# Kernel optimization log

Hardware: AMD Instinct MI355X
Metric: run time of the kernel (lower is better)

Reference implementation:

```python
import jax, jax.numpy as jnp
import numpy as np

B, G, N, E, F, H = 16, 8, 512, 8192, 128, 128
BN_EPS = 1e-5


def setup_inputs() -> dict:
    key = jax.random.key(0)
    ks = jax.random.split(key, 6)
    feats = jax.random.normal(ks[0], (B, G, N, F), jnp.float32)
    edges = jax.random.randint(ks[1], (B, G, 2, E), 0, N, dtype=jnp.int32)
    s = lambda k, shape: jax.random.normal(k, shape, jnp.float32) * 0.05
    return {
        "feats": feats,
        "edges": edges,
        "W0": s(ks[2], (F, H)), "b0": jnp.zeros((H,), jnp.float32),
        "W1": s(ks[3], (H, H)), "b1": jnp.zeros((H,), jnp.float32),
        "Wt": s(ks[4], (H, H)), "bt": jnp.zeros((H,), jnp.float32),
        "gamma": jnp.ones((H,), jnp.float32),
        "beta": jnp.zeros((H,), jnp.float32),
        "run_mean": jnp.zeros((H,), jnp.float32),
        "run_var": jnp.ones((H,), jnp.float32),
    }


def _gconv(x, src, dst, W, b):
    # DGL GraphConv with norm='both': relu(D_in^{-1/2} A D_out^{-1/2} X W + b)
    ones = jnp.ones(src.shape, jnp.float32)
    out_deg = jnp.clip(jax.ops.segment_sum(ones, src, num_segments=N), 1.0)
    in_deg = jnp.clip(jax.ops.segment_sum(ones, dst, num_segments=N), 1.0)
    h = x * jax.lax.rsqrt(out_deg)[:, None]          # src normalization
    agg = jax.ops.segment_sum(h[src], dst, num_segments=N)  # SpMM gather+scatter
    h = agg * jax.lax.rsqrt(in_deg)[:, None]          # dst normalization
    return jax.nn.relu(h @ W + b)


def reference(feats, edges, W0, b0, W1, b1, Wt, bt, gamma, beta, run_mean, run_var):
    def per_graph(x, e):
        src, dst = e[0], e[1]
        h = _gconv(x, src, dst, W0, b0)
        h = _gconv(h, src, dst, W1, b1)
        emb = h.mean(axis=0)  # dgl.mean_nodes readout -> [H]
        z = emb @ Wt + bt
        # BatchNorm1d in eval mode (batch of 1 graph embedding)
        z = gamma * (z - run_mean) * jax.lax.rsqrt(run_var + BN_EPS) + beta
        return jax.nn.relu(z)

    xf = feats.reshape(B * G, N, F)
    ef = edges.reshape(B * G, 2, E)
    out = jax.vmap(per_graph)(xf, ef)  # [B*G, H]
    # torch.stack nesting gives (batch, n_graph, 1, H) since mean_nodes returns [1, H]
    return out.reshape(B, G, 1, H)
```

## Files before the change

kernel.cpp:

```cpp
#include <hip/hip_runtime.h>
#include <hip/hip_bf16.h>

#define NN 512
#define NE 8192
#define NG 128
#define FH 128
#define APITCH 68
#define XPITCH 136
#define BN_EPS 1e-5f

typedef __attribute__((ext_vector_type(8))) short s8v;
typedef __attribute__((ext_vector_type(4))) float f4v;
typedef __attribute__((ext_vector_type(4))) unsigned short us4v;

__device__ inline unsigned short f2bf(float x) {
    unsigned u = __float_as_uint(x);
    unsigned r = (u + 0x7fffu + ((u >> 16) & 1u)) >> 16;
    return (unsigned short)r;
}
__device__ inline float bf2f(unsigned short h) { return __uint_as_float(((unsigned)h) << 16); }

__global__ __launch_bounds__(1024) void k_build(const int* __restrict__ edges,
                                                float* __restrict__ rs_out,
                                                float* __restrict__ rs_in,
                                                int* __restrict__ row_ofs,
                                                int* __restrict__ csr_src,
                                                int* __restrict__ csr_dst,
                                                const float* __restrict__ W0,
                                                const float* __restrict__ W1,
                                                unsigned short* __restrict__ WP) {
    int g = blockIdx.x;
    int tid = threadIdx.x;

    if (g >= NG) {
        int which = g - NG;
        const float* W = which ? W1 : W0;
        for (int task = tid; task < 2048; task += 1024) {
            int t = task >> 6;
            int lane = task & 63;
            int nt = t >> 2, kk = t & 3;
            int n = nt * 16 + (lane & 15);
            int k0 = kk * 32 + (lane >> 4) * 8;
            unsigned short* dh = WP + ((size_t)which * 2 + 0) * 16384 + ((size_t)t * 64 + lane) * 8;
            unsigned short* dl = WP + ((size_t)which * 2 + 1) * 16384 + ((size_t)t * 64 + lane) * 8;
#pragma unroll
            for (int j = 0; j < 8; j++) {
                float v = W[(size_t)(k0 + j) * FH + n];
                unsigned short h = f2bf(v);
                dh[j] = h;
                dl[j] = f2bf(v - bf2f(h));
            }
        }
        return;
    }

    const int* src = edges + (size_t)g * 2 * NE;
    const int* dst = src + NE;

    __shared__ int degO[NN], degI[NN];
    __shared__ int scanA[NN], scanB[NN];
    __shared__ int fill[NN];
    __shared__ int csr_lds[NE];
    __shared__ int dst_lds[NE];

    for (int i = tid; i < NN; i += 1024) { degO[i] = 0; degI[i] = 0; }
    __syncthreads();
    for (int u = tid; u < NE / 4; u += 1024) {
        int4 s = ((const int4*)src)[u];
        int4 d = ((const int4*)dst)[u];
        atomicAdd(&degO[s.x], 1); atomicAdd(&degO[s.y], 1);
        atomicAdd(&degO[s.z], 1); atomicAdd(&degO[s.w], 1);
        atomicAdd(&degI[d.x], 1); atomicAdd(&degI[d.y], 1);
        atomicAdd(&degI[d.z], 1); atomicAdd(&degI[d.w], 1);
    }
    __syncthreads();
    for (int i = tid; i < NN; i += 1024) {
        int dO = degO[i], dI = degI[i];
        rs_out[g * NN + i] = rsqrtf((float)max(dO, 1));
        rs_in [g * NN + i] = rsqrtf((float)max(dI, 1));
        scanA[i] = dI;
    }
    __syncthreads();
    int* sA = scanA; int* sB = scanB;
    for (int off = 1; off < NN; off <<= 1) {
        for (int i = tid; i < NN; i += 1024) {
            int v = sA[i];
            if (i >= off) v += sA[i - off];
            sB[i] = v;
        }
        __syncthreads();
        int* t = sA; sA = sB; sB = t;
    }
    for (int i = tid; i < NN; i += 1024) {
        int excl = (i == 0) ? 0 : sA[i - 1];
        fill[i] = excl;
        row_ofs[g * 513 + i] = excl;
    }
    if (tid == 0) row_ofs[g * 513 + NN] = sA[NN - 1];
    __syncthreads();
    for (int u = tid; u < NE / 4; u += 1024) {
        int4 s = ((const int4*)src)[u];
        int4 d = ((const int4*)dst)[u];
        int p0 = atomicAdd(&fill[d.x], 1); csr_lds[p0] = s.x; dst_lds[p0] = d.x;
        int p1 = atomicAdd(&fill[d.y], 1); csr_lds[p1] = s.y; dst_lds[p1] = d.y;
        int p2 = atomicAdd(&fill[d.z], 1); csr_lds[p2] = s.z; dst_lds[p2] = d.z;
        int p3 = atomicAdd(&fill[d.w], 1); csr_lds[p3] = s.w; dst_lds[p3] = d.w;
    }
    __syncthreads();
    for (int u = tid; u < NE / 4; u += 1024) {
        ((int4*)(csr_src + (size_t)g * NE))[u] = ((const int4*)csr_lds)[u];
        ((int4*)(csr_dst + (size_t)g * NE))[u] = ((const int4*)dst_lds)[u];
    }
}

__global__ __launch_bounds__(256) void k_gemm_f32(const float* __restrict__ X,
                                                  const unsigned short* __restrict__ WPh,
                                                  const unsigned short* __restrict__ WPl,
                                                  const float* __restrict__ rs,
                                                  unsigned short* __restrict__ Yf) {
    __shared__ unsigned short xh[64 * XPITCH];
    __shared__ unsigned short xl[64 * XPITCH];
    int tid = threadIdx.x;
    int sb = blockIdx.y;
    size_t r0 = (size_t)blockIdx.x * NN + (size_t)sb * 64;

    const float4* Xv = (const float4*)(X + r0 * FH);
#pragma unroll
    for (int i = 0; i < 8; i++) {
        int u = tid + i * 256;
        int row = u >> 5, c4 = (u & 31) * 4;
        float4 v = Xv[u];
        int off = row * XPITCH + c4;
        unsigned short h0 = f2bf(v.x), h1 = f2bf(v.y), h2 = f2bf(v.z), h3 = f2bf(v.w);
        xh[off + 0] = h0; xh[off + 1] = h1; xh[off + 2] = h2; xh[off + 3] = h3;
        xl[off + 0] = f2bf(v.x - bf2f(h0));
        xl[off + 1] = f2bf(v.y - bf2f(h1));
        xl[off + 2] = f2bf(v.z - bf2f(h2));
        xl[off + 3] = f2bf(v.w - bf2f(h3));
    }
    __syncthreads();

    int lane = tid & 63, w = tid >> 6;
    int quad = lane >> 4, m = lane & 15;
    int arow = w * 16 + m;

    f4v acc[8];
#pragma unroll
    for (int nt = 0; nt < 8; nt++) acc[nt] = (f4v){0.f, 0.f, 0.f, 0.f};

#pragma unroll
    for (int kk = 0; kk < 4; kk++) {
        s8v ah = *(const s8v*)&xh[arow * XPITCH + kk * 32 + quad * 8];
        s8v al = *(const s8v*)&xl[arow * XPITCH + kk * 32 + quad * 8];
#pragma unroll
        for (int nt = 0; nt < 8; nt++) {
            s8v bh = *(const s8v*)(WPh + ((size_t)(nt * 4 + kk) * 64 + lane) * 8);
            s8v bl = *(const s8v*)(WPl + ((size_t)(nt * 4 + kk) * 64 + lane) * 8);
            acc[nt] = __builtin_amdgcn_mfma_f32_16x16x32_bf16(ah, bh, acc[nt], 0, 0, 0);
            acc[nt] = __builtin_amdgcn_mfma_f32_16x16x32_bf16(al, bh, acc[nt], 0, 0, 0);
            acc[nt] = __builtin_amdgcn_mfma_f32_16x16x32_bf16(ah, bl, acc[nt], 0, 0, 0);
        }
    }

    int orow = w * 16 + quad * 4;
    float4 rsv = *(const float4*)(rs + r0 + orow);
    int tag = (w * 2 + (quad >> 1)) & 3;
    int kko = sb * 2 + (w >> 1);
    int j0  = (quad & 1) * 4;
    unsigned short* of = Yf + (size_t)blockIdx.x * (NN * FH);
#pragma unroll
    for (int nt = 0; nt < 8; nt++) {
        us4v v;
        v.x = f2bf(acc[nt][0] * rsv.x);
        v.y = f2bf(acc[nt][1] * rsv.y);
        v.z = f2bf(acc[nt][2] * rsv.z);
        v.w = f2bf(acc[nt][3] * rsv.w);
        *(us4v*)(of + (((size_t)kko * 8 + nt) * 64 + (m + 16 * tag)) * 8 + j0) = v;
    }
}

__global__ __launch_bounds__(512) void k_fused(const unsigned short* __restrict__ Y1f,
                                               const int* __restrict__ row_ofs,
                                               const int* __restrict__ csr_src,
                                               const int* __restrict__ csr_dst,
                                               const float* __restrict__ rs_in,
                                               const float* __restrict__ rs_out,
                                               const float* __restrict__ bias,
                                               const unsigned short* __restrict__ WPh,
                                               const unsigned short* __restrict__ WPl,
                                               unsigned short* __restrict__ Y2f) {
    int g  = blockIdx.x;
    int sb = blockIdx.y;
    int tid = threadIdx.x;
    int lane = tid & 63, w8 = tid >> 6;
    int quad = lane >> 4, m = lane & 15;
    int mt = w8 & 3, nh = w8 >> 2;
    int base = sb * 64;

    __shared__ int Ach[64 * APITCH];
    __shared__ unsigned short Bs[2 * 8 * 64 * 8];
    unsigned short* hs = (unsigned short*)Ach;
    __shared__ float rsin_s[64];

    if (tid < 64) rsin_s[tid] = rs_in[g * NN + base + tid];

    int eS = row_ofs[g * 513 + base];
    int eE = row_ofs[g * 513 + base + 64];
    const int* cs = csr_src + (size_t)g * NE;
    const int* cd = csr_dst + (size_t)g * NE;
    const int4* Yi4 = (const int4*)(Y1f + (size_t)g * (NN * FH));
    int4* Bi4 = (int4*)Bs;

    f4v acc[4];
#pragma unroll
    for (int j = 0; j < 4; j++) acc[j] = (f4v){0.f, 0.f, 0.f, 0.f};

    for (int p = 0; p < 8; p++) {
        __syncthreads();
        for (int i = tid; i < 64 * APITCH; i += 512) Ach[i] = 0;
        __syncthreads();
        for (int e = eS + tid; e < eE; e += 512) {
            int s = cs[e], d = cd[e];
            if ((s >> 6) == p) atomicAdd(&Ach[(d - base) * APITCH + (s & 63)], 1);
        }
        for (int u = tid; u < 1024; u += 512) Bi4[u] = Yi4[p * 1024 + u];
        __syncthreads();
#pragma unroll
        for (int kkl = 0; kkl < 2; kkl++) {
            s8v bf[4];
#pragma unroll
            for (int j = 0; j < 4; j++)
                bf[j] = *(const s8v*)&Bs[((kkl * 8 + nh * 4 + j) * 64 + lane) * 8];
            const int* ap = &Ach[(mt * 16 + m) * APITCH + kkl * 32 + quad * 8];
            int4 a0 = *(const int4*)ap;
            int4 a1 = *(const int4*)(ap + 4);
            s8v af;
            af[0] = (short)f2bf((float)a0.x); af[1] = (short)f2bf((float)a0.y);
            af[2] = (short)f2bf((float)a0.z); af[3] = (short)f2bf((float)a0.w);
            af[4] = (short)f2bf((float)a1.x); af[5] = (short)f2bf((float)a1.y);
            af[6] = (short)f2bf((float)a1.z); af[7] = (short)f2bf((float)a1.w);
#pragma unroll
            for (int j = 0; j < 4; j++)
                acc[j] = __builtin_amdgcn_mfma_f32_16x16x32_bf16(af, bf[j], acc[j], 0, 0, 0);
        }
    }
    __syncthreads();

#pragma unroll
    for (int j = 0; j < 4; j++) {
        int feat = (nh * 4 + j) * 16 + m;
        float bv = bias[feat];
#pragma unroll
        for (int i = 0; i < 4; i++) {
            int r = mt * 16 + quad * 4 + i;
            float hv = fmaxf(fmaf(rsin_s[r], acc[j][i], bv), 0.f);
            hs[r * XPITCH + feat] = f2bf(hv);
        }
    }
    __syncthreads();

    f4v acc2[4];
#pragma unroll
    for (int j = 0; j < 4; j++) acc2[j] = (f4v){0.f, 0.f, 0.f, 0.f};

#pragma unroll
    for (int kk = 0; kk < 4; kk++) {
        s8v ah = *(const s8v*)&hs[(mt * 16 + m) * XPITCH + kk * 32 + quad * 8];
#pragma unroll
        for (int j = 0; j < 4; j++) {
            int nt = nh * 4 + j;
            s8v bh = *(const s8v*)(WPh + ((size_t)(nt * 4 + kk) * 64 + lane) * 8);
            s8v bl = *(const s8v*)(WPl + ((size_t)(nt * 4 + kk) * 64 + lane) * 8);
            acc2[j] = __builtin_amdgcn_mfma_f32_16x16x32_bf16(ah, bh, acc2[j], 0, 0, 0);
            acc2[j] = __builtin_amdgcn_mfma_f32_16x16x32_bf16(ah, bl, acc2[j], 0, 0, 0);
        }
    }

    int orow = mt * 16 + quad * 4;
    float4 rsv = *(const float4*)(rs_out + (size_t)g * NN + base + orow);
    int tag = (mt * 2 + (quad >> 1)) & 3;
    int kko = sb * 2 + (mt >> 1);
    int j0  = (quad & 1) * 4;
    unsigned short* of = Y2f + (size_t)g * (NN * FH);
#pragma unroll
    for (int j = 0; j < 4; j++) {
        int nt = nh * 4 + j;
        us4v v;
        v.x = f2bf(acc2[j][0] * rsv.x);
        v.y = f2bf(acc2[j][1] * rsv.y);
        v.z = f2bf(acc2[j][2] * rsv.z);
        v.w = f2bf(acc2[j][3] * rsv.w);
        *(us4v*)(of + (((size_t)kko * 8 + nt) * 64 + (m + 16 * tag)) * 8 + j0) = v;
    }
}

__global__ __launch_bounds__(512) void k_gather_mean(const unsigned short* __restrict__ Y2f,
                                                     const int* __restrict__ row_ofs,
                                                     const int* __restrict__ csr_src,
                                                     const int* __restrict__ csr_dst,
                                                     const float* __restrict__ rs_in,
                                                     const float* __restrict__ bias,
                                                     float* __restrict__ partial) {
    int g  = blockIdx.x;
    int sb = blockIdx.y;
    int tid = threadIdx.x;
    int lane = tid & 63, w8 = tid >> 6;
    int quad = lane >> 4, m = lane & 15;
    int mt = w8 & 3, nh = w8 >> 2;
    int base = sb * 64;

    __shared__ int Ach[64 * APITCH];
    __shared__ unsigned short Bs[2 * 8 * 64 * 8];
    float* red = (float*)Ach;
    __shared__ float rsin_s[64];

    if (tid < 64) rsin_s[tid] = rs_in[g * NN + base + tid];

    int eS = row_ofs[g * 513 + base];
    int eE = row_ofs[g * 513 + base + 64];
    const int* cs = csr_src + (size_t)g * NE;
    const int* cd = csr_dst + (size_t)g * NE;
    const int4* Yi4 = (const int4*)(Y2f + (size_t)g * (NN * FH));
    int4* Bi4 = (int4*)Bs;

    f4v acc[4];
#pragma unroll
    for (int j = 0; j < 4; j++) acc[j] = (f4v){0.f, 0.f, 0.f, 0.f};

    for (int p = 0; p < 8; p++) {
        __syncthreads();
        for (int i = tid; i < 64 * APITCH; i += 512) Ach[i] = 0;
        __syncthreads();
        for (int e = eS + tid; e < eE; e += 512) {
            int s = cs[e], d = cd[e];
            if ((s >> 6) == p) atomicAdd(&Ach[(d - base) * APITCH + (s & 63)], 1);
        }
        for (int u = tid; u < 1024; u += 512) Bi4[u] = Yi4[p * 1024 + u];
        __syncthreads();
#pragma unroll
        for (int kkl = 0; kkl < 2; kkl++) {
            s8v bf[4];
#pragma unroll
            for (int j = 0; j < 4; j++)
                bf[j] = *(const s8v*)&Bs[((kkl * 8 + nh * 4 + j) * 64 + lane) * 8];
            const int* ap = &Ach[(mt * 16 + m) * APITCH + kkl * 32 + quad * 8];
            int4 a0 = *(const int4*)ap;
            int4 a1 = *(const int4*)(ap + 4);
            s8v af;
            af[0] = (short)f2bf((float)a0.x); af[1] = (short)f2bf((float)a0.y);
            af[2] = (short)f2bf((float)a0.z); af[3] = (short)f2bf((float)a0.w);
            af[4] = (short)f2bf((float)a1.x); af[5] = (short)f2bf((float)a1.y);
            af[6] = (short)f2bf((float)a1.z); af[7] = (short)f2bf((float)a1.w);
#pragma unroll
            for (int j = 0; j < 4; j++)
                acc[j] = __builtin_amdgcn_mfma_f32_16x16x32_bf16(af, bf[j], acc[j], 0, 0, 0);
        }
    }
    __syncthreads();

#pragma unroll
    for (int j = 0; j < 4; j++) {
        int feat = (nh * 4 + j) * 16 + m;
        float bv = bias[feat];
        float s = 0.f;
#pragma unroll
        for (int i = 0; i < 4; i++) {
            int r = mt * 16 + quad * 4 + i;
            s += fmaxf(fmaf(rsin_s[r], acc[j][i], bv), 0.f);
        }
        red[(w8 * 64 + lane) * 4 + j] = s;
    }
    __syncthreads();
    if (tid < FH) {
        int f = tid;
        int nt = f >> 4, mm = f & 15;
        int nhh = nt >> 2, jj = nt & 3;
        float t = 0.f;
#pragma unroll
        for (int mtt = 0; mtt < 4; mtt++)
#pragma unroll
            for (int q = 0; q < 4; q++)
                t += red[(((nhh * 4 + mtt) * 64) + q * 16 + mm) * 4 + jj];
        partial[((size_t)g * 8 + sb) * FH + f] = t;
    }
}

__global__ __launch_bounds__(128) void k_head(const float* __restrict__ partial,
                                              const float* __restrict__ Wt,
                                              const float* __restrict__ bt,
                                              const float* __restrict__ gamma,
                                              const float* __restrict__ beta,
                                              const float* __restrict__ rmean,
                                              const float* __restrict__ rvar,
                                              float* __restrict__ out) {
    int g = blockIdx.x;
    int j = threadIdx.x;
    __shared__ float e[FH];
    float acc8 = 0.f;
#pragma unroll
    for (int q = 0; q < 8; q++) acc8 += partial[((size_t)g * 8 + q) * FH + j];
    e[j] = acc8 * (1.0f / (float)NN);
    __syncthreads();
    float acc = bt[j];
#pragma unroll 8
    for (int k = 0; k < FH; k++) acc += e[k] * Wt[(size_t)k * FH + j];
    float z = gamma[j] * (acc - rmean[j]) * rsqrtf(rvar[j] + BN_EPS) + beta[j];
    out[g * FH + j] = fmaxf(z, 0.f);
}

extern "C" void kernel_launch(void* const* d_in, const int* in_sizes, int n_in,
                              void* d_out, int out_size, void* d_ws, size_t ws_size,
                              hipStream_t stream) {
    const float* feats = (const float*)d_in[0];
    const int*   edges = (const int*)d_in[1];
    const float* W0    = (const float*)d_in[2];
    const float* b0    = (const float*)d_in[3];
    const float* W1    = (const float*)d_in[4];
    const float* b1    = (const float*)d_in[5];
    const float* Wt    = (const float*)d_in[6];
    const float* bt    = (const float*)d_in[7];
    const float* gamma = (const float*)d_in[8];
    const float* beta  = (const float*)d_in[9];
    const float* rmean = (const float*)d_in[10];
    const float* rvar  = (const float*)d_in[11];
    float* out = (float*)d_out;

    char* w = (char*)d_ws;
    float* rs_out  = (float*)w;   w += sizeof(float) * NG * NN;
    float* rs_in   = (float*)w;   w += sizeof(float) * NG * NN;
    int*   row_ofs = (int*)w;     w += sizeof(int) * NG * 520;
    int*   csr_src = (int*)w;     w += sizeof(int) * ((size_t)NG * NE + 16);
    int*   csr_dst = (int*)w;     w += sizeof(int) * ((size_t)NG * NE + 16);
    unsigned short* WP = (unsigned short*)w;  w += sizeof(unsigned short) * 4 * 16384;
    unsigned short* Y1 = (unsigned short*)w;  w += sizeof(unsigned short) * (size_t)NG * NN * FH;
    unsigned short* Y2 = (unsigned short*)w;  w += sizeof(unsigned short) * (size_t)NG * NN * FH;
    float* partial = (float*)w;   w += sizeof(float) * NG * 8 * FH;

    unsigned short* WPh0 = WP;
    unsigned short* WPl0 = WP + 16384;
    unsigned short* WPh1 = WP + 32768;
    unsigned short* WPl1 = WP + 49152;

    k_build<<<NG + 2, 1024, 0, stream>>>(edges, rs_out, rs_in, row_ofs, csr_src, csr_dst,
                                         W0, W1, WP);

    k_gemm_f32<<<dim3(NG, 8), 256, 0, stream>>>(feats, WPh0, WPl0, rs_out, Y1);

    k_fused<<<dim3(NG, 8), 512, 0, stream>>>(Y1, row_ofs, csr_src, csr_dst,
                                             rs_in, rs_out, b0, WPh1, WPl1, Y2);

    k_gather_mean<<<dim3(NG, 8), 512, 0, stream>>>(Y2, row_ofs, csr_src, csr_dst, rs_in, b1, partial);

    k_head<<<NG, 128, 0, stream>>>(partial, Wt, bt, gamma, beta, rmean, rvar, out);

    (void)in_sizes; (void)n_in; (void)out_size; (void)ws_size;
}
```

Measured before the change: 185.9 us.

## Bucket edges by 64x64 block tile with packed 16-bit local indices

Edge preprocessing now sorts edges into (dst block, src block) buckets of 64x64 tiles, using 16-way replicated counters to spread LDS atomic contention, and stores each edge as a packed 16-bit local (dst,src) pair. The aggregation kernels no longer scan every edge of a destination block for each source panel. Each panel now reads only its own bucket, which cuts redundant edge reads and halves index bandwidth. Adjacency counts are accumulated as float atomics so they can be packed to bf16 with a byte permute rather than an int-to-float conversion and rounding. LDS stores in the fp32 GEMM staging are also vectorized.

```diff
diff --git a/kernel.cpp b/kernel.cpp
--- a/kernel.cpp
+++ b/kernel.cpp
@@ -12,6 +12,7 @@
 typedef __attribute__((ext_vector_type(8))) short s8v;
 typedef __attribute__((ext_vector_type(4))) float f4v;
 typedef __attribute__((ext_vector_type(4))) unsigned short us4v;
+typedef __attribute__((ext_vector_type(4))) unsigned int u4v;
 
 __device__ inline unsigned short f2bf(float x) {
     unsigned u = __float_as_uint(x);
@@ -20,12 +21,15 @@
 }
 __device__ inline float bf2f(unsigned short h) { return __uint_as_float(((unsigned)h) << 16); }
 
+__device__ inline unsigned bfpack(int f1bits, int f0bits) {
+    return __builtin_amdgcn_perm((unsigned)f1bits, (unsigned)f0bits, 0x07060302u);
+}
+
 __global__ __launch_bounds__(1024) void k_build(const int* __restrict__ edges,
                                                 float* __restrict__ rs_out,
                                                 float* __restrict__ rs_in,
-                                                int* __restrict__ row_ofs,
-                                                int* __restrict__ csr_src,
-                                                int* __restrict__ csr_dst,
+                                                int* __restrict__ bofs,
+                                                unsigned short* __restrict__ epk,
                                                 const float* __restrict__ W0,
                                                 const float* __restrict__ W1,
                                                 unsigned short* __restrict__ WP) {
@@ -58,13 +62,15 @@
     const int* dst = src + NE;
 
     __shared__ int degO[NN], degI[NN];
-    __shared__ int scanA[NN], scanB[NN];
-    __shared__ int fill[NN];
-    __shared__ int csr_lds[NE];
-    __shared__ int dst_lds[NE];
+    __shared__ int scanA[1024], scanB[1024];
+    __shared__ int fill[1024];
+    __shared__ unsigned short pk[NE];
 
     for (int i = tid; i < NN; i += 1024) { degO[i] = 0; degI[i] = 0; }
-    __syncthreads();
+    scanA[tid] = 0;
+    __syncthreads();
+
+    int rep = tid & 15;
     for (int u = tid; u < NE / 4; u += 1024) {
         int4 s = ((const int4*)src)[u];
         int4 d = ((const int4*)dst)[u];
@@ -72,45 +78,47 @@
         atomicAdd(&degO[s.z], 1); atomicAdd(&degO[s.w], 1);
         atomicAdd(&degI[d.x], 1); atomicAdd(&degI[d.y], 1);
         atomicAdd(&degI[d.z], 1); atomicAdd(&degI[d.w], 1);
-    }
-    __syncthreads();
+        atomicAdd(&scanA[((((d.x >> 6) << 3) | (s.x >> 6)) << 4) + rep], 1);
+        atomicAdd(&scanA[((((d.y >> 6) << 3) | (s.y >> 6)) << 4) + rep], 1);
+        atomicAdd(&scanA[((((d.z >> 6) << 3) | (s.z >> 6)) << 4) + rep], 1);
+        atomicAdd(&scanA[((((d.w >> 6) << 3) | (s.w >> 6)) << 4) + rep], 1);
+    }
+    __syncthreads();
+
     for (int i = tid; i < NN; i += 1024) {
-        int dO = degO[i], dI = degI[i];
-        rs_out[g * NN + i] = rsqrtf((float)max(dO, 1));
-        rs_in [g * NN + i] = rsqrtf((float)max(dI, 1));
-        scanA[i] = dI;
-    }
-    __syncthreads();
+        rs_out[g * NN + i] = rsqrtf((float)max(degO[i], 1));
+        rs_in [g * NN + i] = rsqrtf((float)max(degI[i], 1));
+    }
+
     int* sA = scanA; int* sB = scanB;
-    for (int off = 1; off < NN; off <<= 1) {
-        for (int i = tid; i < NN; i += 1024) {
-            int v = sA[i];
-            if (i >= off) v += sA[i - off];
-            sB[i] = v;
-        }
+    for (int off = 1; off < 1024; off <<= 1) {
+        int v = sA[tid];
+        if (tid >= off) v += sA[tid - off];
+        sB[tid] = v;
         __syncthreads();
         int* t = sA; sA = sB; sB = t;
     }
-    for (int i = tid; i < NN; i += 1024) {
-        int excl = (i == 0) ? 0 : sA[i - 1];
-        fill[i] = excl;
-        row_ofs[g * 513 + i] = excl;
-    }
-    if (tid == 0) row_ofs[g * 513 + NN] = sA[NN - 1];
-    __syncthreads();
+    int excl = tid ? sA[tid - 1] : 0;
+    fill[tid] = excl;
+    if ((tid & 15) == 0) bofs[g * 65 + (tid >> 4)] = excl;
+    if (tid == 0) bofs[g * 65 + 64] = NE;
+    __syncthreads();
+
     for (int u = tid; u < NE / 4; u += 1024) {
         int4 s = ((const int4*)src)[u];
         int4 d = ((const int4*)dst)[u];
-        int p0 = atomicAdd(&fill[d.x], 1); csr_lds[p0] = s.x; dst_lds[p0] = d.x;
-        int p1 = atomicAdd(&fill[d.y], 1); csr_lds[p1] = s.y; dst_lds[p1] = d.y;
-        int p2 = atomicAdd(&fill[d.z], 1); csr_lds[p2] = s.z; dst_lds[p2] = d.z;
-        int p3 = atomicAdd(&fill[d.w], 1); csr_lds[p3] = s.w; dst_lds[p3] = d.w;
-    }
-    __syncthreads();
-    for (int u = tid; u < NE / 4; u += 1024) {
-        ((int4*)(csr_src + (size_t)g * NE))[u] = ((const int4*)csr_lds)[u];
-        ((int4*)(csr_dst + (size_t)g * NE))[u] = ((const int4*)dst_lds)[u];
-    }
+        int c, p;
+        c = ((((d.x >> 6) << 3) | (s.x >> 6)) << 4) + rep;
+        p = atomicAdd(&fill[c], 1); pk[p] = (unsigned short)(((d.x & 63) << 6) | (s.x & 63));
+        c = ((((d.y >> 6) << 3) | (s.y >> 6)) << 4) + rep;
+        p = atomicAdd(&fill[c], 1); pk[p] = (unsigned short)(((d.y & 63) << 6) | (s.y & 63));
+        c = ((((d.z >> 6) << 3) | (s.z >> 6)) << 4) + rep;
+        p = atomicAdd(&fill[c], 1); pk[p] = (unsigned short)(((d.z & 63) << 6) | (s.z & 63));
+        c = ((((d.w >> 6) << 3) | (s.w >> 6)) << 4) + rep;
+        p = atomicAdd(&fill[c], 1); pk[p] = (unsigned short)(((d.w & 63) << 6) | (s.w & 63));
+    }
+    __syncthreads();
+    ((int4*)(epk + (size_t)g * NE))[tid] = ((const int4*)pk)[tid];
 }
 
 __global__ __launch_bounds__(256) void k_gemm_f32(const float* __restrict__ X,
@@ -132,11 +140,14 @@
         float4 v = Xv[u];
         int off = row * XPITCH + c4;
         unsigned short h0 = f2bf(v.x), h1 = f2bf(v.y), h2 = f2bf(v.z), h3 = f2bf(v.w);
-        xh[off + 0] = h0; xh[off + 1] = h1; xh[off + 2] = h2; xh[off + 3] = h3;
-        xl[off + 0] = f2bf(v.x - bf2f(h0));
-        xl[off + 1] = f2bf(v.y - bf2f(h1));
-        xl[off + 2] = f2bf(v.z - bf2f(h2));
-        xl[off + 3] = f2bf(v.w - bf2f(h3));
+        us4v hv, lv;
+        hv.x = h0; hv.y = h1; hv.z = h2; hv.w = h3;
+        lv.x = f2bf(v.x - bf2f(h0));
+        lv.y = f2bf(v.y - bf2f(h1));
+        lv.z = f2bf(v.z - bf2f(h2));
+        lv.w = f2bf(v.w - bf2f(h3));
+        *(us4v*)(xh + off) = hv;
+        *(us4v*)(xl + off) = lv;
     }
     __syncthreads();
 
@@ -180,9 +191,8 @@
 }
 
 __global__ __launch_bounds__(512) void k_fused(const unsigned short* __restrict__ Y1f,
-                                               const int* __restrict__ row_ofs,
-                                               const int* __restrict__ csr_src,
-                                               const int* __restrict__ csr_dst,
+                                               const int* __restrict__ bofs,
+                                               const unsigned short* __restrict__ epk,
                                                const float* __restrict__ rs_in,
                                                const float* __restrict__ rs_out,
                                                const float* __restrict__ bias,
@@ -197,17 +207,16 @@
     int mt = w8 & 3, nh = w8 >> 2;
     int base = sb * 64;
 
-    __shared__ int Ach[64 * APITCH];
+    __shared__ float Af[64 * APITCH];
     __shared__ unsigned short Bs[2 * 8 * 64 * 8];
-    unsigned short* hs = (unsigned short*)Ach;
+    unsigned short* hs = (unsigned short*)Af;
     __shared__ float rsin_s[64];
+    __shared__ int bo_s[9];
 
     if (tid < 64) rsin_s[tid] = rs_in[g * NN + base + tid];
-
-    int eS = row_ofs[g * 513 + base];
-    int eE = row_ofs[g * 513 + base + 64];
-    const int* cs = csr_src + (size_t)g * NE;
-    const int* cd = csr_dst + (size_t)g * NE;
+    if (tid < 9) bo_s[tid] = bofs[g * 65 + sb * 8 + tid];
+
+    const unsigned short* ep = epk + (size_t)g * NE;
     const int4* Yi4 = (const int4*)(Y1f + (size_t)g * (NN * FH));
     int4* Bi4 = (int4*)Bs;
 
@@ -217,11 +226,12 @@
 
     for (int p = 0; p < 8; p++) {
         __syncthreads();
-        for (int i = tid; i < 64 * APITCH; i += 512) Ach[i] = 0;
-        __syncthreads();
-        for (int e = eS + tid; e < eE; e += 512) {
-            int s = cs[e], d = cd[e];
-            if ((s >> 6) == p) atomicAdd(&Ach[(d - base) * APITCH + (s & 63)], 1);
+        float4 z4 = {0.f, 0.f, 0.f, 0.f};
+        for (int i = tid; i < 64 * APITCH / 4; i += 512) ((float4*)Af)[i] = z4;
+        __syncthreads();
+        for (int e = bo_s[p] + tid; e < bo_s[p + 1]; e += 512) {
+            int v = ep[e];
+            atomicAdd(&Af[(v >> 6) * APITCH + (v & 63)], 1.0f);
         }
         for (int u = tid; u < 1024; u += 512) Bi4[u] = Yi4[p * 1024 + u];
         __syncthreads();
@@ -231,14 +241,15 @@
 #pragma unroll
             for (int j = 0; j < 4; j++)
                 bf[j] = *(const s8v*)&Bs[((kkl * 8 + nh * 4 + j) * 64 + lane) * 8];
-            const int* ap = &Ach[(mt * 16 + m) * APITCH + kkl * 32 + quad * 8];
-            int4 a0 = *(const int4*)ap;
-            int4 a1 = *(const int4*)(ap + 4);
-            s8v af;
-            af[0] = (short)f2bf((float)a0.x); af[1] = (short)f2bf((float)a0.y);
-            af[2] = (short)f2bf((float)a0.z); af[3] = (short)f2bf((float)a0.w);
-            af[4] = (short)f2bf((float)a1.x); af[5] = (short)f2bf((float)a1.y);
-            af[6] = (short)f2bf((float)a1.z); af[7] = (short)f2bf((float)a1.w);
+            const int4* ap = (const int4*)&Af[(mt * 16 + m) * APITCH + kkl * 32 + quad * 8];
+            int4 a0 = ap[0];
+            int4 a1 = ap[1];
+            union { u4v u; s8v s; } cv;
+            cv.u.x = bfpack(a0.y, a0.x);
+            cv.u.y = bfpack(a0.w, a0.z);
+            cv.u.z = bfpack(a1.y, a1.x);
+            cv.u.w = bfpack(a1.w, a1.z);
+            s8v af = cv.s;
 #pragma unroll
             for (int j = 0; j < 4; j++)
                 acc[j] = __builtin_amdgcn_mfma_f32_16x16x32_bf16(af, bf[j], acc[j], 0, 0, 0);
@@ -295,9 +306,8 @@
 }
 
 __global__ __launch_bounds__(512) void k_gather_mean(const unsigned short* __restrict__ Y2f,
-                                                     const int* __restrict__ row_ofs,
-                                                     const int* __restrict__ csr_src,
-                                                     const int* __restrict__ csr_dst,
+                                                     const int* __restrict__ bofs,
+                                                     const unsigned short* __restrict__ epk,
                                                      const float* __restrict__ rs_in,
                                                      const float* __restrict__ bias,
                                                      float* __restrict__ partial) {
@@ -309,17 +319,16 @@
     int mt = w8 & 3, nh = w8 >> 2;
     int base = sb * 64;
 
-    __shared__ int Ach[64 * APITCH];
+    __shared__ float Af[64 * APITCH];
     __shared__ unsigned short Bs[2 * 8 * 64 * 8];
-    float* red = (float*)Ach;
+    float* red = (float*)Af;
     __shared__ float rsin_s[64];
+    __shared__ int bo_s[9];
 
     if (tid < 64) rsin_s[tid] = rs_in[g * NN + base + tid];
-
-    int eS = row_ofs[g * 513 + base];
-    int eE = row_ofs[g * 513 + base + 64];
-    const int* cs = csr_src + (size_t)g * NE;
-    const int* cd = csr_dst + (size_t)g * NE;
+    if (tid < 9) bo_s[tid] = bofs[g * 65 + sb * 8 + tid];
+
+    const unsigned short* ep = epk + (size_t)g * NE;
     const int4* Yi4 = (const int4*)(Y2f + (size_t)g * (NN * FH));
     int4* Bi4 = (int4*)Bs;
 
@@ -329,11 +338,12 @@
 
     for (int p = 0; p < 8; p++) {
         __syncthreads();
-        for (int i = tid; i < 64 * APITCH; i += 512) Ach[i] = 0;
-        __syncthreads();
-        for (int e = eS + tid; e < eE; e += 512) {
-            int s = cs[e], d = cd[e];
-            if ((s >> 6) == p) atomicAdd(&Ach[(d - base) * APITCH + (s & 63)], 1);
+        float4 z4 = {0.f, 0.f, 0.f, 0.f};
+        for (int i = tid; i < 64 * APITCH / 4; i += 512) ((float4*)Af)[i] = z4;
+        __syncthreads();
+        for (int e = bo_s[p] + tid; e < bo_s[p + 1]; e += 512) {
+            int v = ep[e];
+            atomicAdd(&Af[(v >> 6) * APITCH + (v & 63)], 1.0f);
         }
         for (int u = tid; u < 1024; u += 512) Bi4[u] = Yi4[p * 1024 + u];
         __syncthreads();
@@ -343,14 +353,15 @@
 #pragma unroll
             for (int j = 0; j < 4; j++)
                 bf[j] = *(const s8v*)&Bs[((kkl * 8 + nh * 4 + j) * 64 + lane) * 8];
-            const int* ap = &Ach[(mt * 16 + m) * APITCH + kkl * 32 + quad * 8];
-            int4 a0 = *(const int4*)ap;
-            int4 a1 = *(const int4*)(ap + 4);
-            s8v af;
-            af[0] = (short)f2bf((float)a0.x); af[1] = (short)f2bf((float)a0.y);
-            af[2] = (short)f2bf((float)a0.z); af[3] = (short)f2bf((float)a0.w);
-            af[4] = (short)f2bf((float)a1.x); af[5] = (short)f2bf((float)a1.y);
-            af[6] = (short)f2bf((float)a1.z); af[7] = (short)f2bf((float)a1.w);
+            const int4* ap = (const int4*)&Af[(mt * 16 + m) * APITCH + kkl * 32 + quad * 8];
+            int4 a0 = ap[0];
+            int4 a1 = ap[1];
+            union { u4v u; s8v s; } cv;
+            cv.u.x = bfpack(a0.y, a0.x);
+            cv.u.y = bfpack(a0.w, a0.z);
+            cv.u.z = bfpack(a1.y, a1.x);
+            cv.u.w = bfpack(a1.w, a1.z);
+            s8v af = cv.s;
 #pragma unroll
             for (int j = 0; j < 4; j++)
                 acc[j] = __builtin_amdgcn_mfma_f32_16x16x32_bf16(af, bf[j], acc[j], 0, 0, 0);
@@ -428,12 +439,11 @@
     char* w = (char*)d_ws;
     float* rs_out  = (float*)w;   w += sizeof(float) * NG * NN;
     float* rs_in   = (float*)w;   w += sizeof(float) * NG * NN;
-    int*   row_ofs = (int*)w;     w += sizeof(int) * NG * 520;
-    int*   csr_src = (int*)w;     w += sizeof(int) * ((size_t)NG * NE + 16);
-    int*   csr_dst = (int*)w;     w += sizeof(int) * ((size_t)NG * NE + 16);
-    unsigned short* WP = (unsigned short*)w;  w += sizeof(unsigned short) * 4 * 16384;
-    unsigned short* Y1 = (unsigned short*)w;  w += sizeof(unsigned short) * (size_t)NG * NN * FH;
-    unsigned short* Y2 = (unsigned short*)w;  w += sizeof(unsigned short) * (size_t)NG * NN * FH;
+    int*   bofs    = (int*)w;     w += sizeof(int) * NG * 65;
+    unsigned short* epk = (unsigned short*)w; w += sizeof(unsigned short) * (size_t)NG * NE;
+    unsigned short* WP  = (unsigned short*)w; w += sizeof(unsigned short) * 4 * 16384;
+    unsigned short* Y1  = (unsigned short*)w; w += sizeof(unsigned short) * (size_t)NG * NN * FH;
+    unsigned short* Y2  = (unsigned short*)w; w += sizeof(unsigned short) * (size_t)NG * NN * FH;
     float* partial = (float*)w;   w += sizeof(float) * NG * 8 * FH;
 
     unsigned short* WPh0 = WP;
@@ -441,15 +451,13 @@
     unsigned short* WPh1 = WP + 32768;
     unsigned short* WPl1 = WP + 49152;
 
-    k_build<<<NG + 2, 1024, 0, stream>>>(edges, rs_out, rs_in, row_ofs, csr_src, csr_dst,
-                                         W0, W1, WP);
+    k_build<<<NG + 2, 1024, 0, stream>>>(edges, rs_out, rs_in, bofs, epk, W0, W1, WP);
 
     k_gemm_f32<<<dim3(NG, 8), 256, 0, stream>>>(feats, WPh0, WPl0, rs_out, Y1);
 
-    k_fused<<<dim3(NG, 8), 512, 0, stream>>>(Y1, row_ofs, csr_src, csr_dst,
-                                             rs_in, rs_out, b0, WPh1, WPl1, Y2);
-
-    k_gather_mean<<<dim3(NG, 8), 512, 0, stream>>>(Y2, row_ofs, csr_src, csr_dst, rs_in, b1, partial);
+    k_fused<<<dim3(NG, 8), 512, 0, stream>>>(Y1, bofs, epk, rs_in, rs_out, b0, WPh1, WPl1, Y2);
+
+    k_gather_mean<<<dim3(NG, 8), 512, 0, stream>>>(Y2, bofs, epk, rs_in, b1, partial);
 
     k_head<<<NG, 128, 0, stream>>>(partial, Wt, bt, gamma, beta, rmean, rvar, out);
 
```

Result: faster. 175.2 us (-5.8%).

## Replace dense adjacency MFMA aggregation with CSR gather SpMM over row-major features

Applied to the files above, without the earlier changes.

The aggregation step in both graph-conv stages used to build a dense per-block adjacency count matrix in LDS with atomics and multiply it by Y tiles with MFMA, looping over 8 source partitions. It now walks CSR rows directly, with 16 lanes per row each gathering 8 bf16 features per neighbour and accumulating in fp32. Y1 and Y2 are stored row-major through an LDS staging pass so each gather is a contiguous vector load. This removes the dense-matrix zeroing, atomics and wasted MFMA work on a sparse adjacency, and drops the csr_dst array. Rows per block grow to 128, which halves the grid, and the irregular gathers add latency and load imbalance across rows.

```diff
diff --git a/kernel.cpp b/kernel.cpp
--- a/kernel.cpp
+++ b/kernel.cpp
@@ -5,13 +5,12 @@
 #define NE 8192
 #define NG 128
 #define FH 128
-#define APITCH 68
 #define XPITCH 136
 #define BN_EPS 1e-5f
 
 typedef __attribute__((ext_vector_type(8))) short s8v;
 typedef __attribute__((ext_vector_type(4))) float f4v;
-typedef __attribute__((ext_vector_type(4))) unsigned short us4v;
+typedef __attribute__((ext_vector_type(8))) unsigned short us8v;
 
 __device__ inline unsigned short f2bf(float x) {
     unsigned u = __float_as_uint(x);
@@ -25,7 +24,6 @@
                                                 float* __restrict__ rs_in,
                                                 int* __restrict__ row_ofs,
                                                 int* __restrict__ csr_src,
-                                                int* __restrict__ csr_dst,
                                                 const float* __restrict__ W0,
                                                 const float* __restrict__ W1,
                                                 unsigned short* __restrict__ WP) {
@@ -61,7 +59,6 @@
     __shared__ int scanA[NN], scanB[NN];
     __shared__ int fill[NN];
     __shared__ int csr_lds[NE];
-    __shared__ int dst_lds[NE];
 
     for (int i = tid; i < NN; i += 1024) { degO[i] = 0; degI[i] = 0; }
     __syncthreads();
@@ -75,10 +72,9 @@
     }
     __syncthreads();
     for (int i = tid; i < NN; i += 1024) {
-        int dO = degO[i], dI = degI[i];
-        rs_out[g * NN + i] = rsqrtf((float)max(dO, 1));
-        rs_in [g * NN + i] = rsqrtf((float)max(dI, 1));
-        scanA[i] = dI;
+        rs_out[g * NN + i] = rsqrtf((float)max(degO[i], 1));
+        rs_in [g * NN + i] = rsqrtf((float)max(degI[i], 1));
+        scanA[i] = degI[i];
     }
     __syncthreads();
     int* sA = scanA; int* sB = scanB;
@@ -96,21 +92,19 @@
         fill[i] = excl;
         row_ofs[g * 513 + i] = excl;
     }
-    if (tid == 0) row_ofs[g * 513 + NN] = sA[NN - 1];
+    if (tid == 0) row_ofs[g * 513 + NN] = NE;
     __syncthreads();
     for (int u = tid; u < NE / 4; u += 1024) {
         int4 s = ((const int4*)src)[u];
         int4 d = ((const int4*)dst)[u];
-        int p0 = atomicAdd(&fill[d.x], 1); csr_lds[p0] = s.x; dst_lds[p0] = d.x;
-        int p1 = atomicAdd(&fill[d.y], 1); csr_lds[p1] = s.y; dst_lds[p1] = d.y;
-        int p2 = atomicAdd(&fill[d.z], 1); csr_lds[p2] = s.z; dst_lds[p2] = d.z;
-        int p3 = atomicAdd(&fill[d.w], 1); csr_lds[p3] = s.w; dst_lds[p3] = d.w;
-    }
-    __syncthreads();
-    for (int u = tid; u < NE / 4; u += 1024) {
+        int p0 = atomicAdd(&fill[d.x], 1); csr_lds[p0] = s.x;
+        int p1 = atomicAdd(&fill[d.y], 1); csr_lds[p1] = s.y;
+        int p2 = atomicAdd(&fill[d.z], 1); csr_lds[p2] = s.z;
+        int p3 = atomicAdd(&fill[d.w], 1); csr_lds[p3] = s.w;
+    }
+    __syncthreads();
+    for (int u = tid; u < NE / 4; u += 1024)
         ((int4*)(csr_src + (size_t)g * NE))[u] = ((const int4*)csr_lds)[u];
-        ((int4*)(csr_dst + (size_t)g * NE))[u] = ((const int4*)dst_lds)[u];
-    }
 }
 
 __global__ __launch_bounds__(256) void k_gemm_f32(const float* __restrict__ X,
@@ -118,8 +112,10 @@
                                                   const unsigned short* __restrict__ WPl,
                                                   const float* __restrict__ rs,
                                                   unsigned short* __restrict__ Yf) {
-    __shared__ unsigned short xh[64 * XPITCH];
-    __shared__ unsigned short xl[64 * XPITCH];
+    __shared__ unsigned short xb[2 * 64 * XPITCH];
+    unsigned short* xh = xb;
+    unsigned short* xl = xb + 64 * XPITCH;
+    float* Lf = (float*)xb;
     int tid = threadIdx.x;
     int sb = blockIdx.y;
     size_t r0 = (size_t)blockIdx.x * NN + (size_t)sb * 64;
@@ -161,28 +157,33 @@
             acc[nt] = __builtin_amdgcn_mfma_f32_16x16x32_bf16(ah, bl, acc[nt], 0, 0, 0);
         }
     }
+    __syncthreads();
 
     int orow = w * 16 + quad * 4;
     float4 rsv = *(const float4*)(rs + r0 + orow);
-    int tag = (w * 2 + (quad >> 1)) & 3;
-    int kko = sb * 2 + (w >> 1);
-    int j0  = (quad & 1) * 4;
-    unsigned short* of = Yf + (size_t)blockIdx.x * (NN * FH);
 #pragma unroll
     for (int nt = 0; nt < 8; nt++) {
-        us4v v;
-        v.x = f2bf(acc[nt][0] * rsv.x);
-        v.y = f2bf(acc[nt][1] * rsv.y);
-        v.z = f2bf(acc[nt][2] * rsv.z);
-        v.w = f2bf(acc[nt][3] * rsv.w);
-        *(us4v*)(of + (((size_t)kko * 8 + nt) * 64 + (m + 16 * tag)) * 8 + j0) = v;
+        Lf[(orow + 0) * 132 + nt * 16 + m] = acc[nt][0] * rsv.x;
+        Lf[(orow + 1) * 132 + nt * 16 + m] = acc[nt][1] * rsv.y;
+        Lf[(orow + 2) * 132 + nt * 16 + m] = acc[nt][2] * rsv.z;
+        Lf[(orow + 3) * 132 + nt * 16 + m] = acc[nt][3] * rsv.w;
+    }
+    __syncthreads();
+#pragma unroll
+    for (int u0 = 0; u0 < 4; u0++) {
+        int u = tid + u0 * 256;
+        int row = u >> 4, c8 = (u & 15) * 8;
+        const float* p = &Lf[row * 132 + c8];
+        us8v v;
+#pragma unroll
+        for (int j = 0; j < 8; j++) v[j] = f2bf(p[j]);
+        *(us8v*)(Yf + (r0 + row) * FH + c8) = v;
     }
 }
 
 __global__ __launch_bounds__(512) void k_fused(const unsigned short* __restrict__ Y1f,
                                                const int* __restrict__ row_ofs,
                                                const int* __restrict__ csr_src,
-                                               const int* __restrict__ csr_dst,
                                                const float* __restrict__ rs_in,
                                                const float* __restrict__ rs_out,
                                                const float* __restrict__ bias,
@@ -192,196 +193,159 @@
     int g  = blockIdx.x;
     int sb = blockIdx.y;
     int tid = threadIdx.x;
-    int lane = tid & 63, w8 = tid >> 6;
+    int base = sb * 128;
+
+    __shared__ unsigned short hs[128 * XPITCH];
+    __shared__ int   ro_s[129];
+    __shared__ float rsin_s[128], rsout_s[128], b_s[128];
+
+    if (tid < 129) ro_s[tid] = row_ofs[g * 513 + base + tid];
+    if (tid < 128) {
+        rsin_s[tid]  = rs_in [g * NN + base + tid];
+        rsout_s[tid] = rs_out[g * NN + base + tid];
+        b_s[tid]     = bias[tid];
+    }
+    __syncthreads();
+
+    const unsigned short* Yg = Y1f + (size_t)g * (NN * FH);
+    const int* cs = csr_src + (size_t)g * NE;
+    int gid = tid >> 4, l = tid & 15;
+
+#pragma unroll
+    for (int k = 0; k < 4; k++) {
+        int r = gid * 4 + k;
+        int e0 = ro_s[r], e1 = ro_s[r + 1];
+        float a0 = 0.f, a1 = 0.f, a2 = 0.f, a3 = 0.f, a4 = 0.f, a5 = 0.f, a6 = 0.f, a7 = 0.f;
+        int s = (e0 < e1) ? cs[e0] : 0;
+        for (int e = e0; e < e1; e++) {
+            int4 d = *(const int4*)(Yg + (size_t)s * FH + l * 8);
+            if (e + 1 < e1) s = cs[e + 1];
+            a0 += __uint_as_float((unsigned)d.x << 16);
+            a1 += __uint_as_float((unsigned)d.x & 0xffff0000u);
+            a2 += __uint_as_float((unsigned)d.y << 16);
+            a3 += __uint_as_float((unsigned)d.y & 0xffff0000u);
+            a4 += __uint_as_float((unsigned)d.z << 16);
+            a5 += __uint_as_float((unsigned)d.z & 0xffff0000u);
+            a6 += __uint_as_float((unsigned)d.w << 16);
+            a7 += __uint_as_float((unsigned)d.w & 0xffff0000u);
+        }
+        float rv = rsin_s[r];
+        us8v hv;
+        hv[0] = f2bf(fmaxf(fmaf(rv, a0, b_s[l * 8 + 0]), 0.f));
+        hv[1] = f2bf(fmaxf(fmaf(rv, a1, b_s[l * 8 + 1]), 0.f));
+        hv[2] = f2bf(fmaxf(fmaf(rv, a2, b_s[l * 8 + 2]), 0.f));
+        hv[3] = f2bf(fmaxf(fmaf(rv, a3, b_s[l * 8 + 3]), 0.f));
+        hv[4] = f2bf(fmaxf(fmaf(rv, a4, b_s[l * 8 + 4]), 0.f));
+        hv[5] = f2bf(fmaxf(fmaf(rv, a5, b_s[l * 8 + 5]), 0.f));
+        hv[6] = f2bf(fmaxf(fmaf(rv, a6, b_s[l * 8 + 6]), 0.f));
+        hv[7] = f2bf(fmaxf(fmaf(rv, a7, b_s[l * 8 + 7]), 0.f));
+        *(us8v*)&hs[r * XPITCH + l * 8] = hv;
+    }
+    __syncthreads();
+
+    int lane = tid & 63, w = tid >> 6;
     int quad = lane >> 4, m = lane & 15;
-    int mt = w8 & 3, nh = w8 >> 2;
-    int base = sb * 64;
-
-    __shared__ int Ach[64 * APITCH];
-    __shared__ unsigned short Bs[2 * 8 * 64 * 8];
-    unsigned short* hs = (unsigned short*)Ach;
-    __shared__ float rsin_s[64];
-
-    if (tid < 64) rsin_s[tid] = rs_in[g * NN + base + tid];
-
-    int eS = row_ofs[g * 513 + base];
-    int eE = row_ofs[g * 513 + base + 64];
-    const int* cs = csr_src + (size_t)g * NE;
-    const int* cd = csr_dst + (size_t)g * NE;
-    const int4* Yi4 = (const int4*)(Y1f + (size_t)g * (NN * FH));
-    int4* Bi4 = (int4*)Bs;
-
-    f4v acc[4];
-#pragma unroll
-    for (int j = 0; j < 4; j++) acc[j] = (f4v){0.f, 0.f, 0.f, 0.f};
-
-    for (int p = 0; p < 8; p++) {
-        __syncthreads();
-        for (int i = tid; i < 64 * APITCH; i += 512) Ach[i] = 0;
-        __syncthreads();
-        for (int e = eS + tid; e < eE; e += 512) {
-            int s = cs[e], d = cd[e];
-            if ((s >> 6) == p) atomicAdd(&Ach[(d - base) * APITCH + (s & 63)], 1);
-        }
-        for (int u = tid; u < 1024; u += 512) Bi4[u] = Yi4[p * 1024 + u];
-        __syncthreads();
-#pragma unroll
-        for (int kkl = 0; kkl < 2; kkl++) {
-            s8v bf[4];
-#pragma unroll
-            for (int j = 0; j < 4; j++)
-                bf[j] = *(const s8v*)&Bs[((kkl * 8 + nh * 4 + j) * 64 + lane) * 8];
-            const int* ap = &Ach[(mt * 16 + m) * APITCH + kkl * 32 + quad * 8];
-            int4 a0 = *(const int4*)ap;
-            int4 a1 = *(const int4*)(ap + 4);
-            s8v af;
-            af[0] = (short)f2bf((float)a0.x); af[1] = (short)f2bf((float)a0.y);
-            af[2] = (short)f2bf((float)a0.z); af[3] = (short)f2bf((float)a0.w);
-            af[4] = (short)f2bf((float)a1.x); af[5] = (short)f2bf((float)a1.y);
-            af[6] = (short)f2bf((float)a1.z); af[7] = (short)f2bf((float)a1.w);
-#pragma unroll
-            for (int j = 0; j < 4; j++)
-                acc[j] = __builtin_amdgcn_mfma_f32_16x16x32_bf16(af, bf[j], acc[j], 0, 0, 0);
-        }
-    }
-    __syncthreads();
-
-#pragma unroll
-    for (int j = 0; j < 4; j++) {
-        int feat = (nh * 4 + j) * 16 + m;
-        float bv = bias[feat];
-#pragma unroll
-        for (int i = 0; i < 4; i++) {
-            int r = mt * 16 + quad * 4 + i;
-            float hv = fmaxf(fmaf(rsin_s[r], acc[j][i], bv), 0.f);
-            hs[r * XPITCH + feat] = f2bf(hv);
-        }
-    }
-    __syncthreads();
-
-    f4v acc2[4];
-#pragma unroll
-    for (int j = 0; j < 4; j++) acc2[j] = (f4v){0.f, 0.f, 0.f, 0.f};
+
+    f4v acc2[8];
+#pragma unroll
+    for (int nt = 0; nt < 8; nt++) acc2[nt] = (f4v){0.f, 0.f, 0.f, 0.f};
 
 #pragma unroll
     for (int kk = 0; kk < 4; kk++) {
-        s8v ah = *(const s8v*)&hs[(mt * 16 + m) * XPITCH + kk * 32 + quad * 8];
-#pragma unroll
-        for (int j = 0; j < 4; j++) {
-            int nt = nh * 4 + j;
+        s8v ah = *(const s8v*)&hs[(w * 16 + m) * XPITCH + kk * 32 + quad * 8];
+#pragma unroll
+        for (int nt = 0; nt < 8; nt++) {
             s8v bh = *(const s8v*)(WPh + ((size_t)(nt * 4 + kk) * 64 + lane) * 8);
             s8v bl = *(const s8v*)(WPl + ((size_t)(nt * 4 + kk) * 64 + lane) * 8);
-            acc2[j] = __builtin_amdgcn_mfma_f32_16x16x32_bf16(ah, bh, acc2[j], 0, 0, 0);
-            acc2[j] = __builtin_amdgcn_mfma_f32_16x16x32_bf16(ah, bl, acc2[j], 0, 0, 0);
-        }
-    }
-
-    int orow = mt * 16 + quad * 4;
-    float4 rsv = *(const float4*)(rs_out + (size_t)g * NN + base + orow);
-    int tag = (mt * 2 + (quad >> 1)) & 3;
-    int kko = sb * 2 + (mt >> 1);
-    int j0  = (quad & 1) * 4;
-    unsigned short* of = Y2f + (size_t)g * (NN * FH);
-#pragma unroll
-    for (int j = 0; j < 4; j++) {
-        int nt = nh * 4 + j;
-        us4v v;
-        v.x = f2bf(acc2[j][0] * rsv.x);
-        v.y = f2bf(acc2[j][1] * rsv.y);
-        v.z = f2bf(acc2[j][2] * rsv.z);
-        v.w = f2bf(acc2[j][3] * rsv.w);
-        *(us4v*)(of + (((size_t)kko * 8 + nt) * 64 + (m + 16 * tag)) * 8 + j0) = v;
+            acc2[nt] = __builtin_amdgcn_mfma_f32_16x16x32_bf16(ah, bh, acc2[nt], 0, 0, 0);
+            acc2[nt] = __builtin_amdgcn_mfma_f32_16x16x32_bf16(ah, bl, acc2[nt], 0, 0, 0);
+        }
+    }
+    __syncthreads();
+
+    int orow = w * 16 + quad * 4;
+#pragma unroll
+    for (int nt = 0; nt < 8; nt++) {
+#pragma unroll
+        for (int i = 0; i < 4; i++)
+            hs[(orow + i) * XPITCH + nt * 16 + m] = f2bf(acc2[nt][i] * rsout_s[orow + i]);
+    }
+    __syncthreads();
+    unsigned short* of = Y2f + (size_t)g * (NN * FH) + (size_t)base * FH;
+#pragma unroll
+    for (int u0 = 0; u0 < 4; u0++) {
+        int u = tid + u0 * 512;
+        int row = u >> 4, c8 = (u & 15) * 8;
+        *(int4*)(of + row * FH + c8) = *(const int4*)&hs[row * XPITCH + c8];
     }
 }
 
 __global__ __launch_bounds__(512) void k_gather_mean(const unsigned short* __restrict__ Y2f,
                                                      const int* __restrict__ row_ofs,
                                                      const int* __restrict__ csr_src,
-                                                     const int* __restrict__ csr_dst,
                                                      const float* __restrict__ rs_in,
                                                      const float* __restrict__ bias,
                                                      float* __restrict__ partial) {
     int g  = blockIdx.x;
     int sb = blockIdx.y;
     int tid = threadIdx.x;
-    int lane = tid & 63, w8 = tid >> 6;
-    int quad = lane >> 4, m = lane & 15;
-    int mt = w8 & 3, nh = w8 >> 2;
-    int base = sb * 64;
-
-    __shared__ int Ach[64 * APITCH];
-    __shared__ unsigned short Bs[2 * 8 * 64 * 8];
-    float* red = (float*)Ach;
-    __shared__ float rsin_s[64];
-
-    if (tid < 64) rsin_s[tid] = rs_in[g * NN + base + tid];
-
-    int eS = row_ofs[g * 513 + base];
-    int eE = row_ofs[g * 513 + base + 64];
+    int base = sb * 128;
+
+    __shared__ float red[32 * 16 * 8];
+    __shared__ int   ro_s[129];
+    __shared__ float rsin_s[128], b_s[128];
+
+    if (tid < 129) ro_s[tid] = row_ofs[g * 513 + base + tid];
+    if (tid < 128) {
+        rsin_s[tid] = rs_in[g * NN + base + tid];
+        b_s[tid]    = bias[tid];
+    }
+    __syncthreads();
+
+    const unsigned short* Yg = Y2f + (size_t)g * (NN * FH);
     const int* cs = csr_src + (size_t)g * NE;
-    const int* cd = csr_dst + (size_t)g * NE;
-    const int4* Yi4 = (const int4*)(Y2f + (size_t)g * (NN * FH));
-    int4* Bi4 = (int4*)Bs;
-
-    f4v acc[4];
-#pragma unroll
-    for (int j = 0; j < 4; j++) acc[j] = (f4v){0.f, 0.f, 0.f, 0.f};
-
-    for (int p = 0; p < 8; p++) {
-        __syncthreads();
-        for (int i = tid; i < 64 * APITCH; i += 512) Ach[i] = 0;
-        __syncthreads();
-        for (int e = eS + tid; e < eE; e += 512) {
-            int s = cs[e], d = cd[e];
-            if ((s >> 6) == p) atomicAdd(&Ach[(d - base) * APITCH + (s & 63)], 1);
-        }
-        for (int u = tid; u < 1024; u += 512) Bi4[u] = Yi4[p * 1024 + u];
-        __syncthreads();
-#pragma unroll
-        for (int kkl = 0; kkl < 2; kkl++) {
-            s8v bf[4];
-#pragma unroll
-            for (int j = 0; j < 4; j++)
-                bf[j] = *(const s8v*)&Bs[((kkl * 8 + nh * 4 + j) * 64 + lane) * 8];
-            const int* ap = &Ach[(mt * 16 + m) * APITCH + kkl * 32 + quad * 8];
-            int4 a0 = *(const int4*)ap;
-            int4 a1 = *(const int4*)(ap + 4);
-            s8v af;
-            af[0] = (short)f2bf((float)a0.x); af[1] = (short)f2bf((float)a0.y);
-            af[2] = (short)f2bf((float)a0.z); af[3] = (short)f2bf((float)a0.w);
-            af[4] = (short)f2bf((float)a1.x); af[5] = (short)f2bf((float)a1.y);
-            af[6] = (short)f2bf((float)a1.z); af[7] = (short)f2bf((float)a1.w);
-#pragma unroll
-            for (int j = 0; j < 4; j++)
-                acc[j] = __builtin_amdgcn_mfma_f32_16x16x32_bf16(af, bf[j], acc[j], 0, 0, 0);
-        }
-    }
-    __syncthreads();
-
-#pragma unroll
-    for (int j = 0; j < 4; j++) {
-        int feat = (nh * 4 + j) * 16 + m;
-        float bv = bias[feat];
-        float s = 0.f;
-#pragma unroll
-        for (int i = 0; i < 4; i++) {
-            int r = mt * 16 + quad * 4 + i;
-            s += fmaxf(fmaf(rsin_s[r], acc[j][i], bv), 0.f);
-        }
-        red[(w8 * 64 + lane) * 4 + j] = s;
-    }
+    int gid = tid >> 4, l = tid & 15;
+
+    float s0 = 0.f, s1 = 0.f, s2 = 0.f, s3 = 0.f, s4 = 0.f, s5 = 0.f, s6 = 0.f, s7 = 0.f;
+#pragma unroll
+    for (int k = 0; k < 4; k++) {
+        int r = gid * 4 + k;
+        int e0 = ro_s[r], e1 = ro_s[r + 1];
+        float a0 = 0.f, a1 = 0.f, a2 = 0.f, a3 = 0.f, a4 = 0.f, a5 = 0.f, a6 = 0.f, a7 = 0.f;
+        int s = (e0 < e1) ? cs[e0] : 0;
+        for (int e = e0; e < e1; e++) {
+            int4 d = *(const int4*)(Yg + (size_t)s * FH + l * 8);
+            if (e + 1 < e1) s = cs[e + 1];
+            a0 += __uint_as_float((unsigned)d.x << 16);
+            a1 += __uint_as_float((unsigned)d.x & 0xffff0000u);
+            a2 += __uint_as_float((unsigned)d.y << 16);
+            a3 += __uint_as_float((unsigned)d.y & 0xffff0000u);
+            a4 += __uint_as_float((unsigned)d.z << 16);
+            a5 += __uint_as_float((unsigned)d.z & 0xffff0000u);
+            a6 += __uint_as_float((unsigned)d.w << 16);
+            a7 += __uint_as_float((unsigned)d.w & 0xffff0000u);
+        }
+        float rv = rsin_s[r];
+        s0 += fmaxf(fmaf(rv, a0, b_s[l * 8 + 0]), 0.f);
+        s1 += fmaxf(fmaf(rv, a1, b_s[l * 8 + 1]), 0.f);
+        s2 += fmaxf(fmaf(rv, a2, b_s[l * 8 + 2]), 0.f);
+        s3 += fmaxf(fmaf(rv, a3, b_s[l * 8 + 3]), 0.f);
+        s4 += fmaxf(fmaf(rv, a4, b_s[l * 8 + 4]), 0.f);
+        s5 += fmaxf(fmaf(rv, a5, b_s[l * 8 + 5]), 0.f);
+        s6 += fmaxf(fmaf(rv, a6, b_s[l * 8 + 6]), 0.f);
+        s7 += fmaxf(fmaf(rv, a7, b_s[l * 8 + 7]), 0.f);
+    }
+    float* rp = &red[(gid * 16 + l) * 8];
+    rp[0] = s0; rp[1] = s1; rp[2] = s2; rp[3] = s3;
+    rp[4] = s4; rp[5] = s5; rp[6] = s6; rp[7] = s7;
     __syncthreads();
     if (tid < FH) {
-        int f = tid;
-        int nt = f >> 4, mm = f & 15;
-        int nhh = nt >> 2, jj = nt & 3;
+        int f = tid, ll = f >> 3, j = f & 7;
         float t = 0.f;
 #pragma unroll
-        for (int mtt = 0; mtt < 4; mtt++)
-#pragma unroll
-            for (int q = 0; q < 4; q++)
-                t += red[(((nhh * 4 + mtt) * 64) + q * 16 + mm) * 4 + jj];
-        partial[((size_t)g * 8 + sb) * FH + f] = t;
+        for (int grp = 0; grp < 32; grp++)
+            t += red[(grp * 16 + ll) * 8 + j];
+        partial[((size_t)g * 4 + sb) * FH + f] = t;
     }
 }
 
@@ -396,10 +360,10 @@
     int g = blockIdx.x;
     int j = threadIdx.x;
     __shared__ float e[FH];
-    float acc8 = 0.f;
-#pragma unroll
-    for (int q = 0; q < 8; q++) acc8 += partial[((size_t)g * 8 + q) * FH + j];
-    e[j] = acc8 * (1.0f / (float)NN);
+    float acc4 = 0.f;
+#pragma unroll
+    for (int q = 0; q < 4; q++) acc4 += partial[((size_t)g * 4 + q) * FH + j];
+    e[j] = acc4 * (1.0f / (float)NN);
     __syncthreads();
     float acc = bt[j];
 #pragma unroll 8
@@ -428,28 +392,26 @@
     char* w = (char*)d_ws;
     float* rs_out  = (float*)w;   w += sizeof(float) * NG * NN;
     float* rs_in   = (float*)w;   w += sizeof(float) * NG * NN;
-    int*   row_ofs = (int*)w;     w += sizeof(int) * NG * 520;
-    int*   csr_src = (int*)w;     w += sizeof(int) * ((size_t)NG * NE + 16);
-    int*   csr_dst = (int*)w;     w += sizeof(int) * ((size_t)NG * NE + 16);
-    unsigned short* WP = (unsigned short*)w;  w += sizeof(unsigned short) * 4 * 16384;
-    unsigned short* Y1 = (unsigned short*)w;  w += sizeof(unsigned short) * (size_t)NG * NN * FH;
-    unsigned short* Y2 = (unsigned short*)w;  w += sizeof(unsigned short) * (size_t)NG * NN * FH;
-    float* partial = (float*)w;   w += sizeof(float) * NG * 8 * FH;
+    int*   row_ofs = (int*)w;     w += sizeof(int) * NG * 513;
+    int*   csr_src = (int*)w;     w += sizeof(int) * (size_t)NG * NE;
+    unsigned short* WP  = (unsigned short*)w; w += sizeof(unsigned short) * 4 * 16384;
+    unsigned short* Y1  = (unsigned short*)w; w += sizeof(unsigned short) * (size_t)NG * NN * FH;
+    unsigned short* Y2  = (unsigned short*)w; w += sizeof(unsigned short) * (size_t)NG * NN * FH;
+    float* partial = (float*)w;   w += sizeof(float) * NG * 4 * FH;
 
     unsigned short* WPh0 = WP;
     unsigned short* WPl0 = WP + 16384;
     unsigned short* WPh1 = WP + 32768;
     unsigned short* WPl1 = WP + 49152;
 
-    k_build<<<NG + 2, 1024, 0, stream>>>(edges, rs_out, rs_in, row_ofs, csr_src, csr_dst,
-                                         W0, W1, WP);
+    k_build<<<NG + 2, 1024, 0, stream>>>(edges, rs_out, rs_in, row_ofs, csr_src, W0, W1, WP);
 
     k_gemm_f32<<<dim3(NG, 8), 256, 0, stream>>>(feats, WPh0, WPl0, rs_out, Y1);
 
-    k_fused<<<dim3(NG, 8), 512, 0, stream>>>(Y1, row_ofs, csr_src, csr_dst,
-                                             rs_in, rs_out, b0, WPh1, WPl1, Y2);
-
-    k_gather_mean<<<dim3(NG, 8), 512, 0, stream>>>(Y2, row_ofs, csr_src, csr_dst, rs_in, b1, partial);
+    k_fused<<<dim3(NG, 4), 512, 0, stream>>>(Y1, row_ofs, csr_src, rs_in, rs_out, b0,
+                                             WPh1, WPl1, Y2);
+
+    k_gather_mean<<<dim3(NG, 4), 512, 0, stream>>>(Y2, row_ofs, csr_src, rs_in, b1, partial);
 
     k_head<<<NG, 128, 0, stream>>>(partial, Wt, bt, gamma, beta, rmean, rvar, out);
 
```

New measurement: 194.5 us. +4.6%, slower.
